# Kernel optimization log

Measured on AMD Instinct MI355X. Metric: run time of the kernel, lower is better.

The kernel has to match this reference:

```python
import jax, jax.numpy as jnp
import numpy as np

N_NODES = 100000
N_EDGES = 1600000
IN_C, HID_C, OUT_C = 128, 128, 64


def setup_inputs() -> dict:
    key = jax.random.key(0)
    ks = jax.random.split(key, 9)
    features = jax.random.normal(ks[0], (N_NODES, IN_C), dtype=jnp.float32)
    src = jax.random.randint(ks[1], (N_EDGES,), 0, N_NODES, dtype=jnp.int32)
    dst = jax.random.randint(ks[2], (N_EDGES,), 0, N_NODES, dtype=jnp.int32)
    def glorot(k, fan_in, fan_out):
        lim = float(np.sqrt(6.0 / (fan_in + fan_out)))
        return jax.random.uniform(k, (fan_in, fan_out), jnp.float32, -lim, lim)
    return {
        "features": features, "src": src, "dst": dst,
        "W1": glorot(ks[3], IN_C, HID_C), "b1": jnp.zeros((HID_C,), jnp.float32),
        "W2": glorot(ks[4], HID_C, HID_C), "b2": jnp.zeros((HID_C,), jnp.float32),
        "W3": glorot(ks[5], HID_C, OUT_C), "b3": jnp.zeros((OUT_C,), jnp.float32),
    }


def _graph_conv(x, src, dst, W, b, inv_sqrt_out, inv_sqrt_in):
    # DGL GraphConv, norm='both': h = D_in^{-1/2} A D_out^{-1/2} (x W) + b
    h = (x * inv_sqrt_out[:, None]) @ W            # [N, out]
    agg = jax.ops.segment_sum(h[src], dst, num_segments=N_NODES)
    return agg * inv_sqrt_in[:, None] + b


def reference(features, src, dst, W1, b1, W2, b2, W3, b3):
    ones = jnp.ones((N_EDGES,), jnp.float32)
    deg_out = jnp.clip(jax.ops.segment_sum(ones, src, num_segments=N_NODES), 1.0)
    deg_in = jnp.clip(jax.ops.segment_sum(ones, dst, num_segments=N_NODES), 1.0)
    iso, isi = deg_out ** -0.5, deg_in ** -0.5
    x = jax.nn.relu(_graph_conv(features, src, dst, W1, b1, iso, isi))
    x = jax.nn.relu(_graph_conv(x, src, dst, W2, b2, iso, isi))
    x = _graph_conv(x, src, dst, W3, b3, iso, isi)
    return jax.nn.log_softmax(x, axis=1)
```

## Files before the change

### kernel.cpp

```cpp
#include <hip/hip_runtime.h>
#include <hip/hip_bf16.h>

#define IN_C 128
#define HID_C 128
#define OUT_C 64

typedef unsigned short u16;
typedef unsigned int   u32;
typedef __attribute__((ext_vector_type(8))) short short8;
typedef __attribute__((ext_vector_type(4))) float f32x4;
typedef __attribute__((ext_vector_type(2))) float f32x2;

__device__ __forceinline__ u16 bf16_bits(float x) {
    __hip_bfloat16 h = __float2bfloat16(x);
    return *(u16*)&h;
}
__device__ __forceinline__ void split_hi_lo(float a, u16& hi, u16& lo) {
    __hip_bfloat16 h = __float2bfloat16(a);
    float hf = __bfloat162float(h);
    __hip_bfloat16 l = __float2bfloat16(a - hf);
    hi = *(u16*)&h; lo = *(u16*)&l;
}
__device__ __forceinline__ void pk_acc(f32x2& acc, u32 v) {
    f32x2 val;
    val.x = __uint_as_float(v << 16);
    val.y = __uint_as_float(v & 0xffff0000u);
    asm("v_pk_add_f32 %0, %0, %1" : "+v"(acc) : "v"(val));
}


__global__ __launch_bounds__(256)
void part_hist2(const int* __restrict__ src, const int* __restrict__ dst,
                int* __restrict__ bh, int E, int K, int NB) {
    const int b = blockIdx.x;
    extern __shared__ int lh[];
    for (int i = threadIdx.x; i < 2 * K; i += 256) lh[i] = 0;
    __syncthreads();
    const int lo = (int)((long long)E * b / NB);
    const int hi = (int)((long long)E * (b + 1) / NB);
    for (int i = lo + threadIdx.x; i < hi; i += 256) {
        int d = __builtin_nontemporal_load(&dst[i]);
        int s = __builtin_nontemporal_load(&src[i]);
        atomicAdd(&lh[d >> 8], 1);
        atomicAdd(&lh[K + (s >> 8)], 1);
    }
    __syncthreads();
    for (int k = threadIdx.x; k < K; k += 256) {
        bh[k * NB + b]            = lh[k];
        bh[(K + k) * NB + b]      = lh[K + k];
    }
}

__global__ __launch_bounds__(256)
void part_scatter2(const int* __restrict__ src, const int* __restrict__ dst,
                   const int* __restrict__ ofs, u32* __restrict__ pairs,
                   int E, int K, int NB) {
    const int b = blockIdx.x;
    extern __shared__ int lcur[];
    for (int k = threadIdx.x; k < 2 * K; k += 256) lcur[k] = ofs[k * NB + b];
    __syncthreads();
    const int lo = (int)((long long)E * b / NB);
    const int hi = (int)((long long)E * (b + 1) / NB);
    for (int i = lo + threadIdx.x; i < hi; i += 256) {
        int d = __builtin_nontemporal_load(&dst[i]);
        int s = __builtin_nontemporal_load(&src[i]);
        int p1 = atomicAdd(&lcur[d >> 8], 1);
        pairs[p1] = ((u32)s << 8) | (u32)(d & 255);
        int p2 = atomicAdd(&lcur[K + (s >> 8)], 1);
        pairs[p2] = (u32)s;
    }
}

__global__ __launch_bounds__(256)
void bucket_count2(const u32* __restrict__ pairs, const int* __restrict__ OFS,
                   int* __restrict__ cnt_in, int* __restrict__ cnt_out,
                   int N, int NB, int K, int E) {
    const int kk = blockIdx.x;
    const bool is_src = kk >= K;
    const int k = is_src ? kk - K : kk;
    const int* ofs = OFS + (is_src ? K * NB : 0);
    int* cnt = is_src ? cnt_out : cnt_in;
    const int cap = is_src ? 2 * E : E;
    __shared__ int lc[256];
    lc[threadIdx.x] = 0;
    __syncthreads();
    const int s0 = ofs[k * NB];
    const int s1 = (k == K - 1) ? cap : ofs[(k + 1) * NB];
    for (int i = s0 + threadIdx.x; i < s1; i += 256)
        atomicAdd(&lc[pairs[i] & 255], 1);
    __syncthreads();
    const int node = k * 256 + threadIdx.x;
    if (node < N) cnt[node] = lc[threadIdx.x];
}

__global__ __launch_bounds__(256)
void bucket_fill(const u32* __restrict__ pairs, const int* __restrict__ ofs,
                 const int* __restrict__ row_start, int* __restrict__ csr,
                 int N, int NB, int K, int E) {
    const int k = blockIdx.x;
    __shared__ int lcur[256];
    const int node = k * 256 + threadIdx.x;
    lcur[threadIdx.x] = (node < N) ? row_start[node] : 0;
    __syncthreads();
    const int s0 = ofs[k * NB];
    const int s1 = (k == K - 1) ? E : ofs[(k + 1) * NB];
    for (int i = s0 + threadIdx.x; i < s1; i += 256) {
        u32 pr = pairs[i];
        int p = atomicAdd(&lcur[pr & 255], 1);
        csr[p] = (int)(pr >> 8);
    }
}


__global__ __launch_bounds__(256)
void scan_pass1(const int* __restrict__ in, int* __restrict__ blocksum, int M) {
    const int b = blockIdx.x, t = threadIdx.x;
    const int base = b * 1024 + t * 4;
    int s = 0;
#pragma unroll
    for (int j = 0; j < 4; ++j) {
        int idx = base + j;
        if (idx < M) s += in[idx];
    }
#pragma unroll
    for (int off = 32; off >= 1; off >>= 1) s += __shfl_xor(s, off);
    __shared__ int wsum[4];
    if ((t & 63) == 0) wsum[t >> 6] = s;
    __syncthreads();
    if (t == 0) blocksum[b] = wsum[0] + wsum[1] + wsum[2] + wsum[3];
}

__global__ __launch_bounds__(1024)
void scan_g2(int* __restrict__ a, int nb) {
    __shared__ int s[1024];
    const int t = threadIdx.x;
    int v = (t < nb) ? a[t] : 0;
    s[t] = v;
    __syncthreads();
    for (int off = 1; off < 1024; off <<= 1) {
        int x = (t >= off) ? s[t - off] : 0;
        __syncthreads();
        s[t] += x;
        __syncthreads();
    }
    if (t < nb) a[t] = s[t] - v;
}

__global__ __launch_bounds__(256)
void scan_g3(const int* __restrict__ in, const int* __restrict__ blockoff,
             int* __restrict__ out, int M) {
    __shared__ int ssum[256];
    const int b = blockIdx.x, t = threadIdx.x;
    const int base = b * 1024 + t * 4;
    int c[4];
#pragma unroll
    for (int j = 0; j < 4; ++j) {
        int idx = base + j;
        c[j] = (idx < M) ? in[idx] : 0;
    }
    const int tot = c[0] + c[1] + c[2] + c[3];
    ssum[t] = tot;
    __syncthreads();
    for (int off = 1; off < 256; off <<= 1) {
        int v = (t >= off) ? ssum[t - off] : 0;
        __syncthreads();
        ssum[t] += v;
        __syncthreads();
    }
    int run = blockoff[b] + ssum[t] - tot;
#pragma unroll
    for (int j = 0; j < 4; ++j) {
        int idx = base + j;
        if (idx < M) { out[idx] = run; run += c[j]; }
    }
}

__global__ __launch_bounds__(256)
void scan_pass3n(const int* __restrict__ cnt_in, const int* __restrict__ cnt_out,
                 const int* __restrict__ OFS, int* __restrict__ row_start,
                 float* __restrict__ iso, float* __restrict__ isi,
                 int N, int E, int NB) {
    __shared__ int ssum[256];
    const int b = blockIdx.x, t = threadIdx.x;
    const int base = b * 1024 + t * 4;
    int c[4];
#pragma unroll
    for (int j = 0; j < 4; ++j) {
        int idx = base + j;
        c[j] = (idx < N) ? cnt_in[idx] : 0;
    }
    const int tot = c[0] + c[1] + c[2] + c[3];
    ssum[t] = tot;
    __syncthreads();
    for (int off = 1; off < 256; off <<= 1) {
        int v = (t >= off) ? ssum[t - off] : 0;
        __syncthreads();
        ssum[t] += v;
        __syncthreads();
    }
    int run = OFS[(b << 2) * NB] + ssum[t] - tot;
#pragma unroll
    for (int j = 0; j < 4; ++j) {
        int idx = base + j;
        if (idx < N) {
            row_start[idx] = run;
            run += c[j];
            int di = c[j] < 1 ? 1 : c[j];
            int co = cnt_out[idx];
            int dd = co < 1 ? 1 : co;
            isi[idx] = rsqrtf((float)di);
            iso[idx] = rsqrtf((float)dd);
        }
    }
    if (b == 0 && t == 0) row_start[N] = E;
}


__global__ __launch_bounds__(128)
void wt_prep_all(const float* __restrict__ W1, const float* __restrict__ W2,
                 const float* __restrict__ W3, u16* __restrict__ Wt1,
                 u16* __restrict__ Wt2, u16* __restrict__ Wt3) {
    const int b = blockIdx.x, k = threadIdx.x;
    if (b < 128)       Wt1[b * 128 + k] = bf16_bits(W1[k * 128 + b]);
    else if (b < 256)  { int c = b - 128; Wt2[c * 128 + k] = bf16_bits(W2[k * 128 + c]); }
    else               { int c = b - 256; Wt3[c * 128 + k] = bf16_bits(W3[k * 64 + c]); }
}

template <int C>
__device__ __forceinline__
void mfma_store(const u16* sAh, const u16* sAl, const u16* __restrict__ Wt,
                u16* __restrict__ H, int row0, int N, int t) {
    constexpr int NT = C / 16;
    const int wid = t >> 6, lane = t & 63;
    const int r0 = wid * 16;
    const int arow = r0 + (lane & 15);
    const int kb = (lane >> 4) * 8;

    f32x4 acc[NT];
#pragma unroll
    for (int i = 0; i < NT; ++i) acc[i] = (f32x4){0.f, 0.f, 0.f, 0.f};

    const u16* wbase = Wt + (size_t)(lane & 15) * 128 + kb;

#pragma unroll
    for (int kk = 0; kk < 4; ++kk) {
        short8 ah = *(const short8*)(&sAh[arow * 136 + kk * 32 + kb]);
        short8 al = *(const short8*)(&sAl[arow * 136 + kk * 32 + kb]);
#pragma unroll
        for (int ct = 0; ct < NT; ++ct) {
            short8 bf = *(const short8*)(wbase + ct * 16 * 128 + kk * 32);
            acc[ct] = __builtin_amdgcn_mfma_f32_16x16x32_bf16(ah, bf, acc[ct], 0, 0, 0);
            acc[ct] = __builtin_amdgcn_mfma_f32_16x16x32_bf16(al, bf, acc[ct], 0, 0, 0);
        }
    }

    const int rbase = row0 + r0 + (lane >> 4) * 4;
#pragma unroll
    for (int ct = 0; ct < NT; ++ct) {
        int gcol = ct * 16 + (lane & 15);
#pragma unroll
        for (int r = 0; r < 4; ++r) {
            int grow = rbase + r;
            if (grow < N) H[(size_t)grow * C + gcol] = bf16_bits(acc[ct][r]);
        }
    }
}


__global__ __launch_bounds__(256)
void gemm1_fused(const float* __restrict__ X, const float* __restrict__ iso,
                 const u16* __restrict__ Wt, u16* __restrict__ H, int N) {
    __shared__ u16 sAh[64 * 136];
    __shared__ u16 sAl[64 * 136];
    const int t = threadIdx.x;
    const int row0 = blockIdx.x * 64;

    for (int i = t; i < 2048; i += 256) {
        int r = i >> 5, kv = (i & 31) << 2;
        int gr = row0 + r;
        if (gr >= N) gr = N - 1;
        float s = iso[gr];
        float4 x = *(const float4*)(X + (size_t)gr * 128 + kv);
        u16 h0, l0, h1, l1, h2, l2, h3, l3;
        split_hi_lo(x.x * s, h0, l0);
        split_hi_lo(x.y * s, h1, l1);
        split_hi_lo(x.z * s, h2, l2);
        split_hi_lo(x.w * s, h3, l3);
        uint2 hp = make_uint2((u32)h0 | ((u32)h1 << 16), (u32)h2 | ((u32)h3 << 16));
        uint2 lp = make_uint2((u32)l0 | ((u32)l1 << 16), (u32)l2 | ((u32)l3 << 16));
        *(uint2*)(&sAh[r * 136 + kv]) = hp;
        *(uint2*)(&sAl[r * 136 + kv]) = lp;
    }
    __syncthreads();
    mfma_store<128>(sAh, sAl, Wt, H, row0, N, t);
}


template <int C>
__global__ __launch_bounds__(256)
void gemm_mfma(const u16* __restrict__ Ah, const u16* __restrict__ Al,
               const u16* __restrict__ Wt, u16* __restrict__ H, int N) {
    __shared__ u16 sAh[64 * 136];
    __shared__ u16 sAl[64 * 136];
    const int t = threadIdx.x;
    const int row0 = blockIdx.x * 64;

    for (int c = t; c < 1024; c += 256) {
        int r = c >> 4, kc = c & 15;
        int gr = row0 + r;
        if (gr >= N) gr = N - 1;
        *(uint4*)(&sAh[r * 136 + kc * 8]) = *(const uint4*)(Ah + (size_t)gr * 128 + kc * 8);
        *(uint4*)(&sAl[r * 136 + kc * 8]) = *(const uint4*)(Al + (size_t)gr * 128 + kc * 8);
    }
    __syncthreads();
    mfma_store<C>(sAh, sAl, Wt, H, row0, N, t);
}


__device__ __forceinline__
f32x2 gather128(const u16* __restrict__ Hin, const int* __restrict__ csr_src,
                int rs, int re, int lane) {
    f32x2 acc; acc.x = 0.f; acc.y = 0.f;
    int e = rs;
    while (e < re) {
        int nloc = re - e;
        if (nloc > 64) nloc = 64;
        int idx = (lane < nloc) ? __builtin_nontemporal_load(&csr_src[e + lane]) : 0;
        int j = 0;
        for (; j + 16 <= nloc; j += 16) {
            u32 v[16];
#pragma unroll
            for (int q = 0; q < 16; ++q) {
                int s = __builtin_amdgcn_readlane(idx, j + q);
                v[q] = *(const u32*)(Hin + (size_t)s * 128 + lane * 2);
            }
#pragma unroll
            for (int q = 0; q < 16; ++q) pk_acc(acc, v[q]);
        }
        for (; j + 4 <= nloc; j += 4) {
            u32 v[4];
#pragma unroll
            for (int q = 0; q < 4; ++q) {
                int s = __builtin_amdgcn_readlane(idx, j + q);
                v[q] = *(const u32*)(Hin + (size_t)s * 128 + lane * 2);
            }
#pragma unroll
            for (int q = 0; q < 4; ++q) pk_acc(acc, v[q]);
        }
        for (; j < nloc; ++j) {
            int s = __builtin_amdgcn_readlane(idx, j);
            pk_acc(acc, *(const u32*)(Hin + (size_t)s * 128 + lane * 2));
        }
        e += nloc;
    }
    return acc;
}


__global__ __launch_bounds__(256)
void agg_relu(const u16* __restrict__ H, const int* __restrict__ row_start,
              const int* __restrict__ csr_src, const float* __restrict__ isi,
              const float* __restrict__ iso, const float* __restrict__ bias,
              u16* __restrict__ Ah, u16* __restrict__ Al, int N) {
    const int wid  = (int)((blockIdx.x * (size_t)blockDim.x + threadIdx.x) >> 6);
    const int lane = threadIdx.x & 63;
    if (wid >= N) return;
    const int rs = row_start[wid];
    const int re = row_start[wid + 1];

    f32x2 acc = gather128(H, csr_src, rs, re, lane);

    float2 b = *(const float2*)(bias + lane * 2);
    const float sc = isi[wid], so = iso[wid];
    float o0 = fmaxf(acc.x * sc + b.x, 0.f) * so;
    float o1 = fmaxf(acc.y * sc + b.y, 0.f) * so;
    u16 h0, l0, h1, l1;
    split_hi_lo(o0, h0, l0);
    split_hi_lo(o1, h1, l1);
    ((u32*)Ah)[(size_t)wid * 64 + lane] = (u32)h0 | ((u32)h1 << 16);
    ((u32*)Al)[(size_t)wid * 64 + lane] = (u32)l0 | ((u32)l1 << 16);
}


__global__ __launch_bounds__(256)
void agg_final(const u16* __restrict__ H, const int* __restrict__ row_start,
               const int* __restrict__ csr_src, const float* __restrict__ isi,
               const float* __restrict__ bias, float* __restrict__ Out, int N) {
    const int wid  = (int)((blockIdx.x * (size_t)blockDim.x + threadIdx.x) >> 6);
    const int lane = threadIdx.x & 63;
    if (wid >= N) return;
    const int rs = row_start[wid];
    const int re = row_start[wid + 1];
    const float sc = isi[wid];

    float a = 0.f;
    int e = rs;
    while (e < re) {
        int nloc = re - e;
        if (nloc > 64) nloc = 64;
        int idx = (lane < nloc) ? __builtin_nontemporal_load(&csr_src[e + lane]) : 0;
        int j = 0;
        for (; j + 16 <= nloc; j += 16) {
            u32 v[16];
#pragma unroll
            for (int q = 0; q < 16; ++q) {
                int s = __builtin_amdgcn_readlane(idx, j + q);
                v[q] = H[(size_t)s * 64 + lane];
            }
#pragma unroll
            for (int q = 0; q < 16; ++q) a += __uint_as_float(v[q] << 16);
        }
        for (; j + 4 <= nloc; j += 4) {
            u32 v[4];
#pragma unroll
            for (int q = 0; q < 4; ++q) {
                int s = __builtin_amdgcn_readlane(idx, j + q);
                v[q] = H[(size_t)s * 64 + lane];
            }
#pragma unroll
            for (int q = 0; q < 4; ++q) a += __uint_as_float(v[q] << 16);
        }
        for (; j < nloc; ++j) {
            int s = __builtin_amdgcn_readlane(idx, j);
            a += __uint_as_float((u32)H[(size_t)s * 64 + lane] << 16);
        }
        e += nloc;
    }
    float v = a * sc + bias[lane];
    float m = v;
#pragma unroll
    for (int off = 32; off >= 1; off >>= 1) m = fmaxf(m, __shfl_xor(m, off));
    float ex = expf(v - m);
    float ss = ex;
#pragma unroll
    for (int off = 32; off >= 1; off >>= 1) ss += __shfl_xor(ss, off);
    v = (v - m) - logf(ss);
    __builtin_nontemporal_store(v, &Out[(size_t)wid * 64 + lane]);
}


extern "C" void kernel_launch(void* const* d_in, const int* in_sizes, int n_in,
                              void* d_out, int out_size, void* d_ws, size_t ws_size,
                              hipStream_t stream) {
    const float* features = (const float*)d_in[0];
    const int*   src      = (const int*)d_in[1];
    const int*   dst      = (const int*)d_in[2];
    const float* W1       = (const float*)d_in[3];
    const float* b1       = (const float*)d_in[4];
    const float* W2       = (const float*)d_in[5];
    const float* b2       = (const float*)d_in[6];
    const float* W3       = (const float*)d_in[7];
    const float* b3       = (const float*)d_in[8];
    float*       out      = (float*)d_out;

    const int N  = in_sizes[0] / IN_C;
    const int E  = in_sizes[1];
    const int K  = (N + 255) >> 8;
    const int NB = 256;
    const int M  = 2 * K * NB;
    const int nbe = (M + 1023) / 1024;
    const int nb  = (N + 1023) / 1024;

    char* ws = (char*)d_ws;
    const size_t SLOT = 400128;
    int*   cnt_out   = (int*)(ws + 0 * SLOT);
    int*   cnt_in    = (int*)(ws + 1 * SLOT);
    int*   row_start = (int*)(ws + 2 * SLOT);
    float* iso       = (float*)(ws + 3 * SLOT);
    float* isi       = (float*)(ws + 4 * SLOT);
    int*   eblocksum = (int*)(ws + 5 * SLOT);
    int*   csr       = (int*)(ws + 6 * SLOT);
    char*  p         = ws + 6 * SLOT + 6400000;
    int*   BH        = (int*)p;
    int*   OFS       = (int*)(p + 1000000);
    u32*   pairs     = (u32*)(p + 2000000);
    u16*   Hb        = (u16*)(p + 14800000);
    u16*   Ah        = (u16*)(p + 40400000);
    u16*   Al        = (u16*)(p + 66000000);
    u16*   Wt1       = (u16*)(p + 91600000);
    u16*   Wt2       = Wt1 + 128 * 128;
    u16*   Wt3       = Wt2 + 128 * 128;

    const size_t ldsK2 = (size_t)(2 * K) * sizeof(int);

    part_hist2<<<NB, 256, ldsK2, stream>>>(src, dst, BH, E, K, NB);
    scan_pass1<<<nbe, 256, 0, stream>>>(BH, eblocksum, M);
    scan_g2<<<1, 1024, 0, stream>>>(eblocksum, nbe);
    scan_g3<<<nbe, 256, 0, stream>>>(BH, eblocksum, OFS, M);
    part_scatter2<<<NB, 256, ldsK2, stream>>>(src, dst, OFS, pairs, E, K, NB);
    bucket_count2<<<2 * K, 256, 0, stream>>>(pairs, OFS, cnt_in, cnt_out, N, NB, K, E);
    scan_pass3n<<<nb, 256, 0, stream>>>(cnt_in, cnt_out, OFS, row_start, iso, isi, N, E, NB);
    bucket_fill<<<K, 256, 0, stream>>>(pairs, OFS, row_start, csr, N, NB, K, E);

    wt_prep_all<<<320, 128, 0, stream>>>(W1, W2, W3, Wt1, Wt2, Wt3);

    const int gblocks = (N + 63) / 64;
    const int ablocks = (int)(((size_t)N * 64 + 255) / 256);

    gemm1_fused<<<gblocks, 256, 0, stream>>>(features, iso, Wt1, Hb, N);
    agg_relu<<<ablocks, 256, 0, stream>>>(Hb, row_start, csr, isi, iso, b1, Ah, Al, N);
    gemm_mfma<128><<<gblocks, 256, 0, stream>>>(Ah, Al, Wt2, Hb, N);
    agg_relu<<<ablocks, 256, 0, stream>>>(Hb, row_start, csr, isi, iso, b2, Ah, Al, N);
    gemm_mfma<64><<<gblocks, 256, 0, stream>>>(Ah, Al, Wt3, Hb, N);
    agg_final<<<ablocks, 256, 0, stream>>>(Hb, row_start, csr, isi, b3, out, N);
}
```

Before: 378.2 us.

## Pad CSR rows to multiples of four and gather 16-byte row chunks per sub-wave

```diff
diff --git a/kernel.cpp b/kernel.cpp
--- a/kernel.cpp
+++ b/kernel.cpp
@@ -109,6 +109,11 @@
         int p = atomicAdd(&lcur[pr & 255], 1);
         csr[p] = (int)(pr >> 8);
     }
+    __syncthreads();
+    if (node < N) {
+        int end = row_start[node + 1];
+        for (int q = lcur[threadIdx.x]; q < end; ++q) csr[q] = N;
+    }
 }
 
 
@@ -121,6 +126,24 @@
     for (int j = 0; j < 4; ++j) {
         int idx = base + j;
         if (idx < M) s += in[idx];
+    }
+#pragma unroll
+    for (int off = 32; off >= 1; off >>= 1) s += __shfl_xor(s, off);
+    __shared__ int wsum[4];
+    if ((t & 63) == 0) wsum[t >> 6] = s;
+    __syncthreads();
+    if (t == 0) blocksum[b] = wsum[0] + wsum[1] + wsum[2] + wsum[3];
+}
+
+__global__ __launch_bounds__(256)
+void scan_pass1p(const int* __restrict__ in, int* __restrict__ blocksum, int M) {
+    const int b = blockIdx.x, t = threadIdx.x;
+    const int base = b * 1024 + t * 4;
+    int s = 0;
+#pragma unroll
+    for (int j = 0; j < 4; ++j) {
+        int idx = base + j;
+        if (idx < M) s += (in[idx] + 3) & ~3;
     }
 #pragma unroll
     for (int off = 32; off >= 1; off >>= 1) s += __shfl_xor(s, off);
@@ -177,9 +200,8 @@
 
 __global__ __launch_bounds__(256)
 void scan_pass3n(const int* __restrict__ cnt_in, const int* __restrict__ cnt_out,
-                 const int* __restrict__ OFS, int* __restrict__ row_start,
-                 float* __restrict__ iso, float* __restrict__ isi,
-                 int N, int E, int NB) {
+                 const int* __restrict__ blockoff, int* __restrict__ row_start,
+                 float* __restrict__ iso, float* __restrict__ isi, int N) {
     __shared__ int ssum[256];
     const int b = blockIdx.x, t = threadIdx.x;
     const int base = b * 1024 + t * 4;
@@ -189,7 +211,7 @@
         int idx = base + j;
         c[j] = (idx < N) ? cnt_in[idx] : 0;
     }
-    const int tot = c[0] + c[1] + c[2] + c[3];
+    const int tot = ((c[0] + 3) & ~3) + ((c[1] + 3) & ~3) + ((c[2] + 3) & ~3) + ((c[3] + 3) & ~3);
     ssum[t] = tot;
     __syncthreads();
     for (int off = 1; off < 256; off <<= 1) {
@@ -198,21 +220,21 @@
         ssum[t] += v;
         __syncthreads();
     }
-    int run = OFS[(b << 2) * NB] + ssum[t] - tot;
+    int run = blockoff[b] + ssum[t] - tot;
 #pragma unroll
     for (int j = 0; j < 4; ++j) {
         int idx = base + j;
         if (idx < N) {
             row_start[idx] = run;
-            run += c[j];
+            run += (c[j] + 3) & ~3;
             int di = c[j] < 1 ? 1 : c[j];
             int co = cnt_out[idx];
             int dd = co < 1 ? 1 : co;
             isi[idx] = rsqrtf((float)di);
             iso[idx] = rsqrtf((float)dd);
-        }
-    }
-    if (b == 0 && t == 0) row_start[N] = E;
+            if (idx == N - 1) row_start[N] = run;
+        }
+    }
 }
 
 
@@ -274,6 +296,8 @@
     __shared__ u16 sAl[64 * 136];
     const int t = threadIdx.x;
     const int row0 = blockIdx.x * 64;
+
+    if (blockIdx.x == 0 && t < 64) ((u32*)H)[(size_t)N * 64 + t] = 0;
 
     for (int i = t; i < 2048; i += 256) {
         int r = i >> 5, kv = (i & 31) << 2;
@@ -305,6 +329,8 @@
     const int t = threadIdx.x;
     const int row0 = blockIdx.x * 64;
 
+    if (blockIdx.x == 0 && t < C / 2) ((u32*)H)[(size_t)N * (C / 2) + t] = 0;
+
     for (int c = t; c < 1024; c += 256) {
         int r = c >> 4, kc = c & 15;
         int gr = row0 + r;
@@ -318,42 +344,37 @@
 
 
 __device__ __forceinline__
-f32x2 gather128(const u16* __restrict__ Hin, const int* __restrict__ csr_src,
-                int rs, int re, int lane) {
-    f32x2 acc; acc.x = 0.f; acc.y = 0.f;
+void gather128w(const u16* __restrict__ Hin, const int* __restrict__ csr,
+                int rs, int re, int lane, f32x2* acc) {
+    const int sub = lane >> 4;
+    const int cb  = (lane & 15) * 8;
     int e = rs;
     while (e < re) {
         int nloc = re - e;
         if (nloc > 64) nloc = 64;
-        int idx = (lane < nloc) ? __builtin_nontemporal_load(&csr_src[e + lane]) : 0;
+        int idx = (lane < nloc) ? __builtin_nontemporal_load(&csr[e + lane]) : 0;
         int j = 0;
         for (; j + 16 <= nloc; j += 16) {
-            u32 v[16];
-#pragma unroll
-            for (int q = 0; q < 16; ++q) {
-                int s = __builtin_amdgcn_readlane(idx, j + q);
-                v[q] = *(const u32*)(Hin + (size_t)s * 128 + lane * 2);
-            }
-#pragma unroll
-            for (int q = 0; q < 16; ++q) pk_acc(acc, v[q]);
-        }
-        for (; j + 4 <= nloc; j += 4) {
-            u32 v[4];
-#pragma unroll
-            for (int q = 0; q < 4; ++q) {
-                int s = __builtin_amdgcn_readlane(idx, j + q);
-                v[q] = *(const u32*)(Hin + (size_t)s * 128 + lane * 2);
-            }
-#pragma unroll
-            for (int q = 0; q < 4; ++q) pk_acc(acc, v[q]);
-        }
-        for (; j < nloc; ++j) {
-            int s = __builtin_amdgcn_readlane(idx, j);
-            pk_acc(acc, *(const u32*)(Hin + (size_t)s * 128 + lane * 2));
+            int r0 = __shfl(idx, j + sub);
+            int r1 = __shfl(idx, j + 4 + sub);
+            int r2 = __shfl(idx, j + 8 + sub);
+            int r3 = __shfl(idx, j + 12 + sub);
+            uint4 v0 = *(const uint4*)(Hin + (size_t)r0 * 128 + cb);
+            uint4 v1 = *(const uint4*)(Hin + (size_t)r1 * 128 + cb);
+            uint4 v2 = *(const uint4*)(Hin + (size_t)r2 * 128 + cb);
+            uint4 v3 = *(const uint4*)(Hin + (size_t)r3 * 128 + cb);
+            pk_acc(acc[0], v0.x); pk_acc(acc[1], v0.y); pk_acc(acc[2], v0.z); pk_acc(acc[3], v0.w);
+            pk_acc(acc[0], v1.x); pk_acc(acc[1], v1.y); pk_acc(acc[2], v1.z); pk_acc(acc[3], v1.w);
+            pk_acc(acc[0], v2.x); pk_acc(acc[1], v2.y); pk_acc(acc[2], v2.z); pk_acc(acc[3], v2.w);
+            pk_acc(acc[0], v3.x); pk_acc(acc[1], v3.y); pk_acc(acc[2], v3.z); pk_acc(acc[3], v3.w);
+        }
+        for (; j < nloc; j += 4) {
+            int r0 = __shfl(idx, j + sub);
+            uint4 v0 = *(const uint4*)(Hin + (size_t)r0 * 128 + cb);
+            pk_acc(acc[0], v0.x); pk_acc(acc[1], v0.y); pk_acc(acc[2], v0.z); pk_acc(acc[3], v0.w);
         }
         e += nloc;
     }
-    return acc;
 }
 
 
@@ -368,17 +389,38 @@
     const int rs = row_start[wid];
     const int re = row_start[wid + 1];
 
-    f32x2 acc = gather128(H, csr_src, rs, re, lane);
-
-    float2 b = *(const float2*)(bias + lane * 2);
-    const float sc = isi[wid], so = iso[wid];
-    float o0 = fmaxf(acc.x * sc + b.x, 0.f) * so;
-    float o1 = fmaxf(acc.y * sc + b.y, 0.f) * so;
-    u16 h0, l0, h1, l1;
-    split_hi_lo(o0, h0, l0);
-    split_hi_lo(o1, h1, l1);
-    ((u32*)Ah)[(size_t)wid * 64 + lane] = (u32)h0 | ((u32)h1 << 16);
-    ((u32*)Al)[(size_t)wid * 64 + lane] = (u32)l0 | ((u32)l1 << 16);
+    f32x2 acc[4];
+#pragma unroll
+    for (int i = 0; i < 4; ++i) { acc[i].x = 0.f; acc[i].y = 0.f; }
+    gather128w(H, csr_src, rs, re, lane, acc);
+
+#pragma unroll
+    for (int i = 0; i < 4; ++i) {
+        acc[i].x += __shfl_xor(acc[i].x, 16); acc[i].y += __shfl_xor(acc[i].y, 16);
+        acc[i].x += __shfl_xor(acc[i].x, 32); acc[i].y += __shfl_xor(acc[i].y, 32);
+    }
+
+    if (lane < 16) {
+        const float sc = isi[wid], so = iso[wid];
+        float4 ba = *(const float4*)(bias + lane * 8);
+        float4 bb = *(const float4*)(bias + lane * 8 + 4);
+        float o[8];
+        o[0] = acc[0].x * sc + ba.x; o[1] = acc[0].y * sc + ba.y;
+        o[2] = acc[1].x * sc + ba.z; o[3] = acc[1].y * sc + ba.w;
+        o[4] = acc[2].x * sc + bb.x; o[5] = acc[2].y * sc + bb.y;
+        o[6] = acc[3].x * sc + bb.z; o[7] = acc[3].y * sc + bb.w;
+        u32 hp[4], lp[4];
+#pragma unroll
+        for (int i = 0; i < 4; ++i) {
+            u16 h0, l0, h1, l1;
+            split_hi_lo(fmaxf(o[2 * i], 0.f) * so, h0, l0);
+            split_hi_lo(fmaxf(o[2 * i + 1], 0.f) * so, h1, l1);
+            hp[i] = (u32)h0 | ((u32)h1 << 16);
+            lp[i] = (u32)l0 | ((u32)l1 << 16);
+        }
+        *(uint4*)(Ah + (size_t)wid * 128 + lane * 8) = *(uint4*)hp;
+        *(uint4*)(Al + (size_t)wid * 128 + lane * 8) = *(uint4*)lp;
+    }
 }
 
 
@@ -391,9 +433,11 @@
     if (wid >= N) return;
     const int rs = row_start[wid];
     const int re = row_start[wid + 1];
-    const float sc = isi[wid];
-
-    float a = 0.f;
+    const int sub = lane >> 4;
+    const int cb  = (lane & 15) * 4;
+
+    f32x2 a0, a1;
+    a0.x = a0.y = a1.x = a1.y = 0.f;
     int e = rs;
     while (e < re) {
         int nloc = re - e;
@@ -401,41 +445,49 @@
         int idx = (lane < nloc) ? __builtin_nontemporal_load(&csr_src[e + lane]) : 0;
         int j = 0;
         for (; j + 16 <= nloc; j += 16) {
-            u32 v[16];
-#pragma unroll
-            for (int q = 0; q < 16; ++q) {
-                int s = __builtin_amdgcn_readlane(idx, j + q);
-                v[q] = H[(size_t)s * 64 + lane];
-            }
-#pragma unroll
-            for (int q = 0; q < 16; ++q) a += __uint_as_float(v[q] << 16);
-        }
-        for (; j + 4 <= nloc; j += 4) {
-            u32 v[4];
-#pragma unroll
-            for (int q = 0; q < 4; ++q) {
-                int s = __builtin_amdgcn_readlane(idx, j + q);
-                v[q] = H[(size_t)s * 64 + lane];
-            }
-#pragma unroll
-            for (int q = 0; q < 4; ++q) a += __uint_as_float(v[q] << 16);
-        }
-        for (; j < nloc; ++j) {
-            int s = __builtin_amdgcn_readlane(idx, j);
-            a += __uint_as_float((u32)H[(size_t)s * 64 + lane] << 16);
+            int r0 = __shfl(idx, j + sub);
+            int r1 = __shfl(idx, j + 4 + sub);
+            int r2 = __shfl(idx, j + 8 + sub);
+            int r3 = __shfl(idx, j + 12 + sub);
+            uint2 v0 = *(const uint2*)(H + (size_t)r0 * 64 + cb);
+            uint2 v1 = *(const uint2*)(H + (size_t)r1 * 64 + cb);
+            uint2 v2 = *(const uint2*)(H + (size_t)r2 * 64 + cb);
+            uint2 v3 = *(const uint2*)(H + (size_t)r3 * 64 + cb);
+            pk_acc(a0, v0.x); pk_acc(a1, v0.y);
+            pk_acc(a0, v1.x); pk_acc(a1, v1.y);
+            pk_acc(a0, v2.x); pk_acc(a1, v2.y);
+            pk_acc(a0, v3.x); pk_acc(a1, v3.y);
+        }
+        for (; j < nloc; j += 4) {
+            int r0 = __shfl(idx, j + sub);
+            uint2 v0 = *(const uint2*)(H + (size_t)r0 * 64 + cb);
+            pk_acc(a0, v0.x); pk_acc(a1, v0.y);
         }
         e += nloc;
     }
-    float v = a * sc + bias[lane];
-    float m = v;
-#pragma unroll
-    for (int off = 32; off >= 1; off >>= 1) m = fmaxf(m, __shfl_xor(m, off));
-    float ex = expf(v - m);
-    float ss = ex;
-#pragma unroll
-    for (int off = 32; off >= 1; off >>= 1) ss += __shfl_xor(ss, off);
-    v = (v - m) - logf(ss);
-    __builtin_nontemporal_store(v, &Out[(size_t)wid * 64 + lane]);
+
+    a0.x += __shfl_xor(a0.x, 16); a0.y += __shfl_xor(a0.y, 16);
+    a0.x += __shfl_xor(a0.x, 32); a0.y += __shfl_xor(a0.y, 32);
+    a1.x += __shfl_xor(a1.x, 16); a1.y += __shfl_xor(a1.y, 16);
+    a1.x += __shfl_xor(a1.x, 32); a1.y += __shfl_xor(a1.y, 32);
+
+    const float sc = isi[wid];
+    float4 b4 = *(const float4*)(bias + (lane & 15) * 4);
+    float v0 = a0.x * sc + b4.x;
+    float v1 = a0.y * sc + b4.y;
+    float v2 = a1.x * sc + b4.z;
+    float v3 = a1.y * sc + b4.w;
+    float m = fmaxf(fmaxf(v0, v1), fmaxf(v2, v3));
+#pragma unroll
+    for (int off = 8; off >= 1; off >>= 1) m = fmaxf(m, __shfl_xor(m, off));
+    float ss = expf(v0 - m) + expf(v1 - m) + expf(v2 - m) + expf(v3 - m);
+#pragma unroll
+    for (int off = 8; off >= 1; off >>= 1) ss += __shfl_xor(ss, off);
+    float lg = m + logf(ss);
+    if (lane < 16) {
+        float4 o = make_float4(v0 - lg, v1 - lg, v2 - lg, v3 - lg);
+        *(float4*)(Out + (size_t)wid * 64 + lane * 4) = o;
+    }
 }
 
 
@@ -468,16 +520,17 @@
     int*   row_start = (int*)(ws + 2 * SLOT);
     float* iso       = (float*)(ws + 3 * SLOT);
     float* isi       = (float*)(ws + 4 * SLOT);
-    int*   eblocksum = (int*)(ws + 5 * SLOT);
+    int*   blocksum  = (int*)(ws + 5 * SLOT);
+    int*   eblocksum = blocksum + 2048;
     int*   csr       = (int*)(ws + 6 * SLOT);
-    char*  p         = ws + 6 * SLOT + 6400000;
+    char*  p         = ws + 6 * SLOT + 8000000;
     int*   BH        = (int*)p;
     int*   OFS       = (int*)(p + 1000000);
     u32*   pairs     = (u32*)(p + 2000000);
     u16*   Hb        = (u16*)(p + 14800000);
-    u16*   Ah        = (u16*)(p + 40400000);
-    u16*   Al        = (u16*)(p + 66000000);
-    u16*   Wt1       = (u16*)(p + 91600000);
+    u16*   Ah        = (u16*)(p + 40500000);
+    u16*   Al        = (u16*)(p + 66100000);
+    u16*   Wt1       = (u16*)(p + 91700000);
     u16*   Wt2       = Wt1 + 128 * 128;
     u16*   Wt3       = Wt2 + 128 * 128;
 
@@ -489,7 +542,9 @@
     scan_g3<<<nbe, 256, 0, stream>>>(BH, eblocksum, OFS, M);
     part_scatter2<<<NB, 256, ldsK2, stream>>>(src, dst, OFS, pairs, E, K, NB);
     bucket_count2<<<2 * K, 256, 0, stream>>>(pairs, OFS, cnt_in, cnt_out, N, NB, K, E);
-    scan_pass3n<<<nb, 256, 0, stream>>>(cnt_in, cnt_out, OFS, row_start, iso, isi, N, E, NB);
+    scan_pass1p<<<nb, 256, 0, stream>>>(cnt_in, blocksum, N);
+    scan_g2<<<1, 1024, 0, stream>>>(blocksum, nb);
+    scan_pass3n<<<nb, 256, 0, stream>>>(cnt_in, cnt_out, blocksum, row_start, iso, isi, N);
     bucket_fill<<<K, 256, 0, stream>>>(pairs, OFS, row_start, csr, N, NB, K, E);
 
     wt_prep_all<<<320, 128, 0, stream>>>(W1, W2, W3, Wt1, Wt2, Wt3);
```

New measurement: 376.5 us. About the same (-0.4%).
